# Optimization experiments

Hardware: AMD Instinct MI355X
Metric: run time of the kernel (lower is better)

Reference implementation:

```python
import jax, jax.numpy as jnp
import numpy as np

C = 256
RED = 8
DQK = C // RED  # 32


def setup_inputs() -> dict:
    key = jax.random.key(0)
    ks = jax.random.split(key, 8)
    B, H, W = 8, 64, 64
    x = jax.random.normal(ks[0], (B, C, H, W), dtype=jnp.float32)
    # 1x1 conv weights stored as [out, in]; biases [out]
    Wq = jax.random.normal(ks[1], (DQK, C), dtype=jnp.float32) * 0.02
    bq = jax.random.normal(ks[2], (DQK,), dtype=jnp.float32) * 0.02
    Wk = jax.random.normal(ks[3], (DQK, C), dtype=jnp.float32) * 0.02
    bk = jax.random.normal(ks[4], (DQK,), dtype=jnp.float32) * 0.02
    Wv = jax.random.normal(ks[5], (C, C), dtype=jnp.float32) * 0.02
    bv = jax.random.normal(ks[6], (C,), dtype=jnp.float32) * 0.02
    gamma = jax.random.normal(ks[7], (1,), dtype=jnp.float32) * 0.1
    return {"x": x, "Wq": Wq, "bq": bq, "Wk": Wk, "bk": bk, "Wv": Wv, "bv": bv, "gamma": gamma}


def reference(x, Wq, bq, Wk, bk, Wv, bv, gamma):
    B, Cc, H, W = x.shape
    N = H * W
    xf = x.reshape(B, Cc, N)                       # (B, C, N)
    # 1x1 convs == per-pixel dense projections
    q = jnp.einsum('dc,bcn->bdn', Wq, xf) + bq[None, :, None]   # (B, d, N)
    k = jnp.einsum('dc,bcn->bdn', Wk, xf) + bk[None, :, None]   # (B, d, N)
    v = jnp.einsum('ec,bcn->ben', Wv, xf) + bv[None, :, None]   # (B, C, N)
    # energy[b,i,j] = q[b,:,i] . k[b,:,j]; softmax over j (no scaling, SAGAN-style)
    energy = jnp.einsum('bdi,bdj->bij', q, k)      # (B, N, N)
    attn = jax.nn.softmax(energy, axis=-1)
    # out[b,c,i] = sum_j v[b,c,j] * attn[b,i,j]
    out = jnp.einsum('bcj,bij->bci', v, attn)      # (B, C, N)
    out = out.reshape(B, Cc, H, W)
    return gamma[0] * out + x
```

## Files before the change

### kernel.cpp

```cpp
#include <hip/hip_runtime.h>

#define NB 8
#define CCH 256
#define DQK 32
#define NPIX 4096

typedef __attribute__((ext_vector_type(8))) short short8;
typedef __attribute__((ext_vector_type(4))) float f32x4;
typedef __attribute__((ext_vector_type(4))) unsigned short ushort4v;

static __device__ __forceinline__ unsigned short f2bf(float f) {
  unsigned int u = __builtin_bit_cast(unsigned int, f);
  u += 0x7FFFu + ((u >> 16) & 1u);
  return (unsigned short)(u >> 16);
}

__global__ __launch_bounds__(256) void wconv_kernel(
    const float* __restrict__ Wq, const float* __restrict__ Wk,
    const float* __restrict__ Wv, unsigned short* __restrict__ Wbf) {
  const int e = (blockIdx.x * 256 + threadIdx.x) * 4;
  const int m = e >> 8, c = e & 255;
  const float* src;
  if (m < 32) src = Wq + (size_t)m * CCH;
  else if (m < 64) src = Wk + (size_t)(m - 32) * CCH;
  else src = Wv + (size_t)(m - 64) * CCH;
  const float4 v = *(const float4*)(src + c);
  ushort4v o;
  o[0] = f2bf(v.x); o[1] = f2bf(v.y); o[2] = f2bf(v.z); o[3] = f2bf(v.w);
  *(ushort4v*)(Wbf + e) = o;
}

__global__ __launch_bounds__(256) void proj_kernel(
    const float* __restrict__ x, const unsigned short* __restrict__ Wbf,
    const float* __restrict__ bq, const float* __restrict__ bk,
    const float* __restrict__ bv,
    unsigned short* __restrict__ Qb, unsigned short* __restrict__ Kb,
    unsigned short* __restrict__ Vb) {
  __shared__ unsigned short xs[64 * 256];
  const int t = threadIdx.x;
  const int b = blockIdx.x >> 6;
  const int i0 = (blockIdx.x & 63) * 64;
  const float* xb = x + (size_t)b * CCH * NPIX + i0;
  {
    const int ii = (t & 15) * 4;
    const int cb = t >> 4;
    const int sw8 = ((ii >> 2) & 7) << 3;
#pragma unroll
    for (int rep = 0; rep < 16; ++rep) {
      const int c = cb + 16 * rep;
      const float4 v = *(const float4*)(xb + (size_t)c * NPIX + ii);
      const float vv[4] = {v.x, v.y, v.z, v.w};
#pragma unroll
      for (int d = 0; d < 4; ++d) {
        const int cc = (c ^ sw8) ^ ((d & 1) << 4);
        xs[(ii + d) * 256 + cc] = f2bf(vv[d]);
      }
    }
  }
  __syncthreads();
  const int w = t >> 6, l = t & 63;
  const int lc = l & 15, lg = l >> 4;
  const int m0w = 80 * w;
  f32x4 acc[5][4];
#pragma unroll
  for (int mt = 0; mt < 5; ++mt)
#pragma unroll
    for (int nt = 0; nt < 4; ++nt) acc[mt][nt] = (f32x4){0.f, 0.f, 0.f, 0.f};

#pragma unroll
  for (int kk = 0; kk < 8; ++kk) {
    short8 af[5];
#pragma unroll
    for (int mt = 0; mt < 5; ++mt)
      af[mt] = *(const short8*)(Wbf + (size_t)(m0w + mt * 16 + lc) * CCH + kk * 32 + lg * 8);
#pragma unroll
    for (int nt = 0; nt < 4; ++nt) {
      const int i = nt * 16 + lc;
      const int s = (4 * nt + (lc >> 2)) & 7;
      const int cc = ((kk * 32 + lg * 8) ^ (s << 3)) ^ ((lc & 1) << 4);
      const short8 bfv = *(const short8*)&xs[i * 256 + cc];
#pragma unroll
      for (int mt = 0; mt < 5; ++mt)
        acc[mt][nt] = __builtin_amdgcn_mfma_f32_16x16x32_bf16(af[mt], bfv, acc[mt][nt], 0, 0, 0);
    }
  }
#pragma unroll
  for (int mt = 0; mt < 5; ++mt) {
    const int mbase = m0w + mt * 16;
    const int mrow = mbase + 4 * lg;
    if (mbase < 64) {
      const float* bias = (mbase < 32) ? (bq + mrow) : (bk + (mrow - 32));
      unsigned short* dst = (mbase < 32) ? (Qb + (size_t)b * NPIX * DQK + mrow)
                                         : (Kb + (size_t)b * NPIX * DQK + (mrow - 32));
      const float b0 = bias[0], b1 = bias[1], b2 = bias[2], b3 = bias[3];
#pragma unroll
      for (int nt = 0; nt < 4; ++nt) {
        const int i = i0 + nt * 16 + lc;
        ushort4v o;
        o[0] = f2bf(acc[mt][nt][0] + b0);
        o[1] = f2bf(acc[mt][nt][1] + b1);
        o[2] = f2bf(acc[mt][nt][2] + b2);
        o[3] = f2bf(acc[mt][nt][3] + b3);
        *(ushort4v*)(dst + (size_t)i * DQK) = o;
      }
    } else {
      const int vrow = mbase - 64 + 4 * lg;
#pragma unroll
      for (int jj = 0; jj < 4; ++jj) {
        const float bias = bv[vrow + jj];
        unsigned short* vdst = Vb + ((size_t)b * CCH + vrow + jj) * NPIX + i0;
#pragma unroll
        for (int nt = 0; nt < 4; ++nt)
          vdst[nt * 16 + lc] = f2bf(acc[mt][nt][jj] + bias);
      }
    }
  }
}

__global__ __launch_bounds__(256) void attn_kernel(
    const unsigned short* __restrict__ Qb,
    const unsigned short* __restrict__ Kb,
    const unsigned short* __restrict__ Vb,
    const float* __restrict__ x,
    const float* __restrict__ gammap,
    float* __restrict__ out) {
  __shared__ unsigned short Plds[64 * 64];
  __shared__ float tsc[4][2][16][17];
  __shared__ float l_lds[64];
  const int t = threadIdx.x;
  const int w = t >> 6, l = t & 63;
  const int lc = l & 15, lg = l >> 4;
  const int b = blockIdx.x >> 6;
  const int q0 = (blockIdx.x & 63) * 64;

  const unsigned short* Qbb = Qb + (size_t)b * NPIX * DQK;
  const unsigned short* Kl = Kb + (size_t)b * NPIX * DQK + (size_t)lc * DQK + lg * 8;
  const unsigned short* Vl = Vb + ((size_t)b * CCH + 64 * w + lc) * NPIX + lg * 8;

  const short8 qa = *(const short8*)(Qbb + (size_t)(q0 + 16 * w + lc) * DQK + lg * 8);
  const f32x4 zero4 = {0.f, 0.f, 0.f, 0.f};

  f32x4 acc[4][4];
#pragma unroll
  for (int mt = 0; mt < 4; ++mt)
#pragma unroll
    for (int ct = 0; ct < 4; ++ct) acc[mt][ct] = (f32x4){0.f, 0.f, 0.f, 0.f};
  float psum[4] = {0.f, 0.f, 0.f, 0.f};
  unsigned short pu[4][4];

#pragma unroll
  for (int kt = 0; kt < 4; ++kt) {
    const short8 kf = *(const short8*)(Kl + (size_t)(kt * 16) * DQK);
    const f32x4 s = __builtin_amdgcn_mfma_f32_16x16x32_bf16(qa, kf, zero4, 0, 0, 0);
#pragma unroll
    for (int jj = 0; jj < 4; ++jj) {
      const float pe = __expf(s[jj]);
      psum[jj] += pe;
      pu[kt][jj] = f2bf(pe);
    }
  }

  for (int ks = 0; ks < 64; ++ks) {
    const int k0 = ks * 64;
#pragma unroll
    for (int kt = 0; kt < 4; ++kt) {
      const int kb = kt * 16 + lc;
#pragma unroll
      for (int jj = 0; jj < 4; ++jj) {
        const int qb = 16 * w + lg * 4 + jj;
        Plds[qb * 64 + (kb ^ ((qb & 7) << 3))] = pu[kt][jj];
      }
    }
    __syncthreads();
    const bool notlast = (ks < 63);
    short8 kfn[4];
    if (notlast) {
#pragma unroll
      for (int kt = 0; kt < 4; ++kt)
        kfn[kt] = *(const short8*)(Kl + (size_t)(k0 + 64 + kt * 16) * DQK);
    }
    short8 vf[2][4];
#pragma unroll
    for (int ks2 = 0; ks2 < 2; ++ks2)
#pragma unroll
      for (int ct = 0; ct < 4; ++ct)
        vf[ks2][ct] = *(const short8*)(Vl + (size_t)(16 * ct) * NPIX + k0 + 32 * ks2);
#pragma unroll
    for (int ks2 = 0; ks2 < 2; ++ks2) {
      short8 pa[4];
#pragma unroll
      for (int mt = 0; mt < 4; ++mt) {
        const int qb = 16 * mt + lc;
        const int ke = 32 * ks2 + 8 * lg;
        pa[mt] = *(const short8*)&Plds[qb * 64 + (ke ^ ((qb & 7) << 3))];
      }
#pragma unroll
      for (int ct = 0; ct < 4; ++ct)
#pragma unroll
        for (int mt = 0; mt < 4; ++mt)
          acc[mt][ct] = __builtin_amdgcn_mfma_f32_16x16x32_bf16(pa[mt], vf[ks2][ct], acc[mt][ct], 0, 0, 0);
    }
    if (notlast) {
#pragma unroll
      for (int kt = 0; kt < 4; ++kt) {
        const f32x4 s = __builtin_amdgcn_mfma_f32_16x16x32_bf16(qa, kfn[kt], zero4, 0, 0, 0);
#pragma unroll
        for (int jj = 0; jj < 4; ++jj) {
          const float pe = __expf(s[jj]);
          psum[jj] += pe;
          pu[kt][jj] = f2bf(pe);
        }
      }
    }
    __syncthreads();
  }

#pragma unroll
  for (int jj = 0; jj < 4; ++jj) {
    float v = psum[jj];
    v += __shfl_xor(v, 1);
    v += __shfl_xor(v, 2);
    v += __shfl_xor(v, 4);
    v += __shfl_xor(v, 8);
    if (lc == 0) l_lds[16 * w + lg * 4 + jj] = v;
  }
  __syncthreads();

  const float g = gammap[0];
  float linv[4][4];
#pragma unroll
  for (int mt = 0; mt < 4; ++mt)
#pragma unroll
    for (int jj = 0; jj < 4; ++jj) linv[mt][jj] = 1.0f / l_lds[16 * mt + lg * 4 + jj];

  const float* xbp = x + (size_t)b * CCH * NPIX;
  float* ob = out + (size_t)b * CCH * NPIX;
#pragma unroll
  for (int mt = 0; mt < 4; ++mt) {
#pragma unroll
    for (int ct = 0; ct < 4; ++ct) {
      const int pb = (mt * 4 + ct) & 1;
#pragma unroll
      for (int jj = 0; jj < 4; ++jj)
        tsc[w][pb][lg * 4 + jj][lc] = g * acc[mt][ct][jj] * linv[mt][jj];
#pragma unroll
      for (int r = 0; r < 4; ++r) {
        const int cl = lg + 4 * r;
        const float v = tsc[w][pb][lc][cl];
        const size_t idx = (size_t)(64 * w + 16 * ct + cl) * NPIX + (size_t)(q0 + 16 * mt + lc);
        ob[idx] = v + xbp[idx];
      }
    }
  }
}

extern "C" void kernel_launch(void* const* d_in, const int* in_sizes, int n_in,
                              void* d_out, int out_size, void* d_ws, size_t ws_size,
                              hipStream_t stream) {
  (void)in_sizes; (void)n_in; (void)out_size; (void)ws_size;
  const float* x     = (const float*)d_in[0];
  const float* Wq    = (const float*)d_in[1];
  const float* bq    = (const float*)d_in[2];
  const float* Wk    = (const float*)d_in[3];
  const float* bk    = (const float*)d_in[4];
  const float* Wv    = (const float*)d_in[5];
  const float* bv    = (const float*)d_in[6];
  const float* gamma = (const float*)d_in[7];

  unsigned short* Wbf = (unsigned short*)d_ws;
  unsigned short* Qb  = Wbf + 320 * CCH;
  unsigned short* Kb  = Qb + (size_t)NB * NPIX * DQK;
  unsigned short* Vb  = Kb + (size_t)NB * NPIX * DQK;

  wconv_kernel<<<80, 256, 0, stream>>>(Wq, Wk, Wv, Wbf);
  proj_kernel<<<512, 256, 0, stream>>>(x, Wbf, bq, bk, bv, Qb, Kb, Vb);
  attn_kernel<<<512, 256, 0, stream>>>(Qb, Kb, Vb, x, gamma, (float*)d_out);
}
```

Before: 270.3 us.

## Double-buffer P tiles and prefetch K/V registers in attention loop

The attention kernel now double-buffers the P tile in shared memory and keeps two register sets for V and K fragments, so loads for the next step are issued before the current PV MFMAs and one barrier per step is removed. The QK MFMA operands are swapped so each lane writes packed bf16 pairs as 8-byte stores, and the row-sum reduction shrinks to two shuffles. The epilogue transposes through padded LDS and uses float4 loads and stores for the residual add. Other changes: launch bounds ask for two blocks per CU, the batch index moves to the low bits of the block id, and the projection kernel uses 32-pixel tiles with twice as many blocks. The extra prefetch registers can raise register pressure and spilling risk.

```diff
diff --git a/kernel.cpp b/kernel.cpp
--- a/kernel.cpp
+++ b/kernel.cpp
@@ -13,6 +13,9 @@
   unsigned int u = __builtin_bit_cast(unsigned int, f);
   u += 0x7FFFu + ((u >> 16) & 1u);
   return (unsigned short)(u >> 16);
+}
+static __device__ __forceinline__ unsigned int pack2bf(float a, float b) {
+  return (unsigned int)f2bf(a) | ((unsigned int)f2bf(b) << 16);
 }
 
 __global__ __launch_bounds__(256) void wconv_kernel(
@@ -36,18 +39,18 @@
     const float* __restrict__ bv,
     unsigned short* __restrict__ Qb, unsigned short* __restrict__ Kb,
     unsigned short* __restrict__ Vb) {
-  __shared__ unsigned short xs[64 * 256];
+  __shared__ unsigned short xs[32 * 256];
   const int t = threadIdx.x;
-  const int b = blockIdx.x >> 6;
-  const int i0 = (blockIdx.x & 63) * 64;
+  const int b = blockIdx.x & 7;
+  const int i0 = (blockIdx.x >> 3) * 32;
   const float* xb = x + (size_t)b * CCH * NPIX + i0;
   {
-    const int ii = (t & 15) * 4;
-    const int cb = t >> 4;
+    const int ii = (t & 7) * 4;
+    const int cb = t >> 3;
     const int sw8 = ((ii >> 2) & 7) << 3;
 #pragma unroll
-    for (int rep = 0; rep < 16; ++rep) {
-      const int c = cb + 16 * rep;
+    for (int rep = 0; rep < 8; ++rep) {
+      const int c = cb + 32 * rep;
       const float4 v = *(const float4*)(xb + (size_t)c * NPIX + ii);
       const float vv[4] = {v.x, v.y, v.z, v.w};
 #pragma unroll
@@ -61,11 +64,11 @@
   const int w = t >> 6, l = t & 63;
   const int lc = l & 15, lg = l >> 4;
   const int m0w = 80 * w;
-  f32x4 acc[5][4];
+  f32x4 acc[5][2];
 #pragma unroll
   for (int mt = 0; mt < 5; ++mt)
 #pragma unroll
-    for (int nt = 0; nt < 4; ++nt) acc[mt][nt] = (f32x4){0.f, 0.f, 0.f, 0.f};
+    for (int nt = 0; nt < 2; ++nt) acc[mt][nt] = (f32x4){0.f, 0.f, 0.f, 0.f};
 
 #pragma unroll
   for (int kk = 0; kk < 8; ++kk) {
@@ -74,7 +77,7 @@
     for (int mt = 0; mt < 5; ++mt)
       af[mt] = *(const short8*)(Wbf + (size_t)(m0w + mt * 16 + lc) * CCH + kk * 32 + lg * 8);
 #pragma unroll
-    for (int nt = 0; nt < 4; ++nt) {
+    for (int nt = 0; nt < 2; ++nt) {
       const int i = nt * 16 + lc;
       const int s = (4 * nt + (lc >> 2)) & 7;
       const int cc = ((kk * 32 + lg * 8) ^ (s << 3)) ^ ((lc & 1) << 4);
@@ -94,7 +97,7 @@
                                          : (Kb + (size_t)b * NPIX * DQK + (mrow - 32));
       const float b0 = bias[0], b1 = bias[1], b2 = bias[2], b3 = bias[3];
 #pragma unroll
-      for (int nt = 0; nt < 4; ++nt) {
+      for (int nt = 0; nt < 2; ++nt) {
         const int i = i0 + nt * 16 + lc;
         ushort4v o;
         o[0] = f2bf(acc[mt][nt][0] + b0);
@@ -110,146 +113,156 @@
         const float bias = bv[vrow + jj];
         unsigned short* vdst = Vb + ((size_t)b * CCH + vrow + jj) * NPIX + i0;
 #pragma unroll
-        for (int nt = 0; nt < 4; ++nt)
+        for (int nt = 0; nt < 2; ++nt)
           vdst[nt * 16 + lc] = f2bf(acc[mt][nt][jj] + bias);
       }
     }
   }
 }
 
-__global__ __launch_bounds__(256) void attn_kernel(
+union AttnSmem {
+  unsigned short p[2][64 * 64];
+  float tsc[4][16 * 68];
+};
+
+__global__ __launch_bounds__(256, 2) void attn_kernel(
     const unsigned short* __restrict__ Qb,
     const unsigned short* __restrict__ Kb,
     const unsigned short* __restrict__ Vb,
     const float* __restrict__ x,
     const float* __restrict__ gammap,
     float* __restrict__ out) {
-  __shared__ unsigned short Plds[64 * 64];
-  __shared__ float tsc[4][2][16][17];
+  __shared__ AttnSmem sm;
   __shared__ float l_lds[64];
   const int t = threadIdx.x;
   const int w = t >> 6, l = t & 63;
   const int lc = l & 15, lg = l >> 4;
-  const int b = blockIdx.x >> 6;
-  const int q0 = (blockIdx.x & 63) * 64;
-
-  const unsigned short* Qbb = Qb + (size_t)b * NPIX * DQK;
+  const int b = blockIdx.x & 7;
+  const int q0 = (blockIdx.x >> 3) * 64;
+
   const unsigned short* Kl = Kb + (size_t)b * NPIX * DQK + (size_t)lc * DQK + lg * 8;
   const unsigned short* Vl = Vb + ((size_t)b * CCH + 64 * w + lc) * NPIX + lg * 8;
-
-  const short8 qa = *(const short8*)(Qbb + (size_t)(q0 + 16 * w + lc) * DQK + lg * 8);
+  const short8 qa = *(const short8*)(Qb + (size_t)b * NPIX * DQK +
+                                     (size_t)(q0 + 16 * w + lc) * DQK + lg * 8);
   const f32x4 zero4 = {0.f, 0.f, 0.f, 0.f};
+  const int pwb = (16 * w + lc) * 128;
+  const int psw = (lc & 7) << 3;
 
   f32x4 acc[4][4];
 #pragma unroll
   for (int mt = 0; mt < 4; ++mt)
 #pragma unroll
     for (int ct = 0; ct < 4; ++ct) acc[mt][ct] = (f32x4){0.f, 0.f, 0.f, 0.f};
-  float psum[4] = {0.f, 0.f, 0.f, 0.f};
-  unsigned short pu[4][4];
-
+  float psum = 0.f;
+
+  short8 vfA[8], vfB[8], kfA[4], kfB[4];
+
+#pragma unroll
+  for (int kt = 0; kt < 4; ++kt)
+    kfA[kt] = *(const short8*)(Kl + (size_t)(kt * 16) * DQK);
 #pragma unroll
   for (int kt = 0; kt < 4; ++kt) {
-    const short8 kf = *(const short8*)(Kl + (size_t)(kt * 16) * DQK);
-    const f32x4 s = __builtin_amdgcn_mfma_f32_16x16x32_bf16(qa, kf, zero4, 0, 0, 0);
-#pragma unroll
-    for (int jj = 0; jj < 4; ++jj) {
-      const float pe = __expf(s[jj]);
-      psum[jj] += pe;
-      pu[kt][jj] = f2bf(pe);
-    }
-  }
-
-  for (int ks = 0; ks < 64; ++ks) {
-    const int k0 = ks * 64;
-#pragma unroll
-    for (int kt = 0; kt < 4; ++kt) {
-      const int kb = kt * 16 + lc;
-#pragma unroll
-      for (int jj = 0; jj < 4; ++jj) {
-        const int qb = 16 * w + lg * 4 + jj;
-        Plds[qb * 64 + (kb ^ ((qb & 7) << 3))] = pu[kt][jj];
-      }
-    }
-    __syncthreads();
-    const bool notlast = (ks < 63);
-    short8 kfn[4];
-    if (notlast) {
-#pragma unroll
-      for (int kt = 0; kt < 4; ++kt)
-        kfn[kt] = *(const short8*)(Kl + (size_t)(k0 + 64 + kt * 16) * DQK);
-    }
-    short8 vf[2][4];
-#pragma unroll
-    for (int ks2 = 0; ks2 < 2; ++ks2)
-#pragma unroll
-      for (int ct = 0; ct < 4; ++ct)
-        vf[ks2][ct] = *(const short8*)(Vl + (size_t)(16 * ct) * NPIX + k0 + 32 * ks2);
-#pragma unroll
-    for (int ks2 = 0; ks2 < 2; ++ks2) {
-      short8 pa[4];
-#pragma unroll
-      for (int mt = 0; mt < 4; ++mt) {
-        const int qb = 16 * mt + lc;
-        const int ke = 32 * ks2 + 8 * lg;
-        pa[mt] = *(const short8*)&Plds[qb * 64 + (ke ^ ((qb & 7) << 3))];
-      }
-#pragma unroll
-      for (int ct = 0; ct < 4; ++ct)
-#pragma unroll
-        for (int mt = 0; mt < 4; ++mt)
-          acc[mt][ct] = __builtin_amdgcn_mfma_f32_16x16x32_bf16(pa[mt], vf[ks2][ct], acc[mt][ct], 0, 0, 0);
-    }
-    if (notlast) {
-#pragma unroll
-      for (int kt = 0; kt < 4; ++kt) {
-        const f32x4 s = __builtin_amdgcn_mfma_f32_16x16x32_bf16(qa, kfn[kt], zero4, 0, 0, 0);
-#pragma unroll
-        for (int jj = 0; jj < 4; ++jj) {
-          const float pe = __expf(s[jj]);
-          psum[jj] += pe;
-          pu[kt][jj] = f2bf(pe);
-        }
-      }
-    }
-    __syncthreads();
-  }
-
-#pragma unroll
-  for (int jj = 0; jj < 4; ++jj) {
-    float v = psum[jj];
-    v += __shfl_xor(v, 1);
-    v += __shfl_xor(v, 2);
-    v += __shfl_xor(v, 4);
-    v += __shfl_xor(v, 8);
-    if (lc == 0) l_lds[16 * w + lg * 4 + jj] = v;
-  }
+    const f32x4 s = __builtin_amdgcn_mfma_f32_16x16x32_bf16(kfA[kt], qa, zero4, 0, 0, 0);
+    const float p0 = __expf(s[0]), p1 = __expf(s[1]);
+    const float p2 = __expf(s[2]), p3 = __expf(s[3]);
+    psum += (p0 + p1) + (p2 + p3);
+    uint2 wv; wv.x = pack2bf(p0, p1); wv.y = pack2bf(p2, p3);
+    *(uint2*)((char*)sm.p[0] + pwb + (((16 * kt + 4 * lg) ^ psw) << 1)) = wv;
+  }
+#pragma unroll
+  for (int ct = 0; ct < 4; ++ct) {
+    vfA[ct] = *(const short8*)(Vl + (size_t)(16 * ct) * NPIX);
+    vfA[4 + ct] = *(const short8*)(Vl + (size_t)(16 * ct) * NPIX + 32);
+  }
+#pragma unroll
+  for (int kt = 0; kt < 4; ++kt)
+    kfB[kt] = *(const short8*)(Kl + (size_t)(64 + kt * 16) * DQK);
   __syncthreads();
 
+#define ATTN_ITER(T, BUF, VF, KF_CUR, VF_NXT, KF_NXT)                               \
+  {                                                                                 \
+    const int t_ = (T);                                                             \
+    if (t_ < 63) {                                                                  \
+      const size_t kb2 = (size_t)(t_ + 1) * 64;                                     \
+      _Pragma("unroll") for (int ct = 0; ct < 4; ++ct) {                            \
+        VF_NXT[ct] = *(const short8*)(Vl + (size_t)(16 * ct) * NPIX + kb2);         \
+        VF_NXT[4 + ct] = *(const short8*)(Vl + (size_t)(16 * ct) * NPIX + kb2 + 32);\
+      }                                                                             \
+      if (t_ < 62) {                                                                \
+        const size_t kk2 = (size_t)(t_ + 2) * 64;                                   \
+        _Pragma("unroll") for (int kt = 0; kt < 4; ++kt)                            \
+          KF_NXT[kt] = *(const short8*)(Kl + (kk2 + kt * 16) * DQK);                \
+      }                                                                             \
+    }                                                                               \
+    unsigned short* pb_ = sm.p[BUF];                                                \
+    unsigned short* pb2_ = sm.p[(BUF) ^ 1];                                         \
+    _Pragma("unroll") for (int ks2 = 0; ks2 < 2; ++ks2) {                           \
+      short8 pa[4];                                                                 \
+      _Pragma("unroll") for (int mt = 0; mt < 4; ++mt)                              \
+        pa[mt] = *(const short8*)((const char*)pb_ + (16 * mt + lc) * 128 +         \
+                                  (((32 * ks2 + 8 * lg) ^ psw) << 1));              \
+      _Pragma("unroll") for (int ct = 0; ct < 4; ++ct)                              \
+        _Pragma("unroll") for (int mt = 0; mt < 4; ++mt)                            \
+          acc[mt][ct] = __builtin_amdgcn_mfma_f32_16x16x32_bf16(                    \
+              pa[mt], VF[ks2 * 4 + ct], acc[mt][ct], 0, 0, 0);                      \
+    }                                                                               \
+    if (t_ < 63) {                                                                  \
+      _Pragma("unroll") for (int kt = 0; kt < 4; ++kt) {                            \
+        const f32x4 s = __builtin_amdgcn_mfma_f32_16x16x32_bf16(                    \
+            KF_CUR[kt], qa, zero4, 0, 0, 0);                                        \
+        const float p0 = __expf(s[0]), p1 = __expf(s[1]);                           \
+        const float p2 = __expf(s[2]), p3 = __expf(s[3]);                           \
+        psum += (p0 + p1) + (p2 + p3);                                              \
+        uint2 wv; wv.x = pack2bf(p0, p1); wv.y = pack2bf(p2, p3);                   \
+        *(uint2*)((char*)pb2_ + pwb + (((16 * kt + 4 * lg) ^ psw) << 1)) = wv;      \
+      }                                                                             \
+    }                                                                               \
+    __syncthreads();                                                                \
+  }
+
+  for (int ks = 0; ks < 64; ks += 2) {
+    ATTN_ITER(ks, 0, vfA, kfB, vfB, kfA);
+    ATTN_ITER(ks + 1, 1, vfB, kfA, vfA, kfB);
+  }
+#undef ATTN_ITER
+
+  {
+    float v = psum;
+    v += __shfl_xor(v, 16);
+    v += __shfl_xor(v, 32);
+    if (l < 16) l_lds[16 * w + lc] = v;
+  }
+  __syncthreads();
+
   const float g = gammap[0];
-  float linv[4][4];
+  float linv4[4][4];
 #pragma unroll
   for (int mt = 0; mt < 4; ++mt)
 #pragma unroll
-    for (int jj = 0; jj < 4; ++jj) linv[mt][jj] = 1.0f / l_lds[16 * mt + lg * 4 + jj];
-
+    for (int jj = 0; jj < 4; ++jj)
+      linv4[mt][jj] = 1.0f / l_lds[16 * mt + 4 * lg + jj];
+
+  float* tw = sm.tsc[w];
   const float* xbp = x + (size_t)b * CCH * NPIX;
   float* ob = out + (size_t)b * CCH * NPIX;
 #pragma unroll
-  for (int mt = 0; mt < 4; ++mt) {
-#pragma unroll
-    for (int ct = 0; ct < 4; ++ct) {
-      const int pb = (mt * 4 + ct) & 1;
-#pragma unroll
-      for (int jj = 0; jj < 4; ++jj)
-        tsc[w][pb][lg * 4 + jj][lc] = g * acc[mt][ct][jj] * linv[mt][jj];
-#pragma unroll
-      for (int r = 0; r < 4; ++r) {
-        const int cl = lg + 4 * r;
-        const float v = tsc[w][pb][lc][cl];
-        const size_t idx = (size_t)(64 * w + 16 * ct + cl) * NPIX + (size_t)(q0 + 16 * mt + lc);
-        ob[idx] = v + xbp[idx];
-      }
+  for (int ct = 0; ct < 4; ++ct) {
+#pragma unroll
+    for (int mt = 0; mt < 4; ++mt) {
+      f32x4 o;
+#pragma unroll
+      for (int jj = 0; jj < 4; ++jj) o[jj] = g * acc[mt][ct][jj] * linv4[mt][jj];
+      *(f32x4*)(tw + lc * 68 + 16 * mt + 4 * lg) = o;
+    }
+#pragma unroll
+    for (int r = 0; r < 4; ++r) {
+      const int crow = 4 * r + lg;
+      const f32x4 o = *(const f32x4*)(tw + crow * 68 + lc * 4);
+      const size_t idx = (size_t)(64 * w + 16 * ct + crow) * NPIX + (size_t)(q0 + lc * 4);
+      const float4 xv = *(const float4*)(xbp + idx);
+      float4 ov;
+      ov.x = o[0] + xv.x; ov.y = o[1] + xv.y; ov.z = o[2] + xv.z; ov.w = o[3] + xv.w;
+      *(float4*)(ob + idx) = ov;
     }
   }
 }
@@ -273,6 +286,6 @@
   unsigned short* Vb  = Kb + (size_t)NB * NPIX * DQK;
 
   wconv_kernel<<<80, 256, 0, stream>>>(Wq, Wk, Wv, Wbf);
-  proj_kernel<<<512, 256, 0, stream>>>(x, Wbf, bq, bk, bv, Qb, Kb, Vb);
+  proj_kernel<<<1024, 256, 0, stream>>>(x, Wbf, bq, bk, bv, Qb, Kb, Vb);
   attn_kernel<<<512, 256, 0, stream>>>(Qb, Kb, Vb, x, gamma, (float*)d_out);
 }
```

New measurement: 272.9 us. About the same (+1.0%).
